# Kernel tuning notes

Measured on AMD Instinct MI355X. Metric: run time of the kernel, lower is better.

The kernel has to match this reference:

```python
import jax, jax.numpy as jnp
import numpy as np

EPS = 1e-8  # matches torch F.cosine_similarity default eps


def _flatten_spatial(x):
    # [B, C, d, h, w] -> [B, N, C]
    B, C = x.shape[:2]
    return x.reshape(B, C, -1).transpose(0, 2, 1)


def _stage_loss(canon_src, canon_tgt, src_desc, tgt_desc):
    stage_size = src_desc.shape[2:]
    B, C = canon_src.shape[:2]
    # trilinear resize with half-pixel centers == torch align_corners=False
    rs = jax.image.resize(canon_src, (B, C) + stage_size, method='trilinear')
    rt = jax.image.resize(canon_tgt, (B, C) + stage_size, method='trilinear')
    a = _flatten_spatial(rs)  # [B, N, 3]
    b = _flatten_spatial(rt)  # [B, N, 3]
    # squared euclidean distances (argmin is invariant to sqrt)
    a2 = jnp.sum(a * a, axis=-1)  # [B, N]
    b2 = jnp.sum(b * b, axis=-1)  # [B, N]
    ab = jnp.einsum('bnc,bmc->bnm', a, b)  # [B, N, N]
    d2 = a2[:, :, None] + b2[:, None, :] - 2.0 * ab
    nearest = jnp.argmin(d2, axis=-1)  # [B, N] int
    sd = _flatten_spatial(src_desc)  # [B, N, Cd]
    td = _flatten_spatial(tgt_desc)  # [B, N, Cd]
    gathered = jnp.take_along_axis(td, nearest[:, :, None], axis=1)  # [B, N, Cd]
    num = jnp.sum(sd * gathered, axis=-1)
    denom = jnp.maximum(jnp.linalg.norm(sd, axis=-1), EPS) * \
            jnp.maximum(jnp.linalg.norm(gathered, axis=-1), EPS)
    cos = num / denom
    return 1.0 - jnp.mean(cos)


def setup_inputs() -> dict:
    key = jax.random.key(0)
    ks = jax.random.split(key, 6)
    return {
        'canonical_source': jax.random.normal(ks[0], (4, 3, 64, 64, 64), jnp.float32),
        'canonical_target': jax.random.normal(ks[1], (4, 3, 64, 64, 64), jnp.float32),
        'src_desc0': jax.random.normal(ks[2], (4, 32, 16, 16, 16), jnp.float32),
        'tgt_desc0': jax.random.normal(ks[3], (4, 32, 16, 16, 16), jnp.float32),
        'src_desc1': jax.random.normal(ks[4], (4, 32, 8, 8, 8), jnp.float32),
        'tgt_desc1': jax.random.normal(ks[5], (4, 32, 8, 8, 8), jnp.float32),
    }


def reference(canonical_source, canonical_target, src_desc0, tgt_desc0, src_desc1, tgt_desc1):
    l0 = _stage_loss(canonical_source, canonical_target, src_desc0, tgt_desc0)
    l1 = _stage_loss(canonical_source, canonical_target, src_desc1, tgt_desc1)
    return jnp.stack([l0, l1]).mean()
```

## Files before the change

kernel.cpp:

```cpp
#include <hip/hip_runtime.h>
#include <cfloat>

typedef unsigned long long u64;

#define CDESC 32
#define N0 4096
#define N1 512

__device__ __forceinline__ unsigned fbits_mono(float d) {
    unsigned b = __float_as_uint(d);
    return (d >= 0.f) ? (b | 0x80000000u) : ~b;
}

__device__ __forceinline__ void wave_reduce_atomic(float v, float* acc) {
#pragma unroll
    for (int off = 32; off > 0; off >>= 1) v += __shfl_down(v, off, 64);
    if ((threadIdx.x & 63) == 0) atomicAdd(acc, v);
}

__global__ __launch_bounds__(256) void pass1_fused(
        const float* __restrict__ csrc, const float* __restrict__ ctgt,
        const float* __restrict__ sd0, const float* __restrict__ td0,
        const float* __restrict__ sd1, const float* __restrict__ td1,
        float* __restrict__ t16a, float* __restrict__ t16b,
        float* __restrict__ t8a,  float* __restrict__ t8b,
        float* __restrict__ sd0T, float* __restrict__ td0T,
        float* __restrict__ sd1T, float* __restrict__ td1T,
        float* __restrict__ acc) {
    __shared__ __align__(16) float sRow[65 * 64];
    const int tid = threadIdx.x;
    const int bx  = blockIdx.x, by = blockIdx.y;
    if (by == 0 && bx == 0 && tid < 4) acc[tid] = 0.f;

    if (bx < 768) {
        int bc = bx >> 6, z = bx & 63;
        const float* in = by ? ctgt : csrc;
        float* o16 = by ? t16b : t16a;
        float* o8  = by ? t8b  : t8a;
        const float4* src = (const float4*)(in + (size_t)(bc * 64 + z) * 4096);
#pragma unroll
        for (int k = 0; k < 4; ++k) {
            float4 v = src[tid + k * 256];
            int g = tid + k * 256;
            int y = g >> 4, j = (g & 15) * 4;
            float* p = &sRow[y * 65 + j];
            p[0] = v.x; p[1] = v.y; p[2] = v.z; p[3] = v.w;
        }
        __syncthreads();
#pragma unroll
        for (int k = 0; k < 6; ++k) {
            int o = tid + k * 256;
            if (o < 1024) {
                int y = o >> 4, xo = o & 15;
                int j0 = 4 * xo - 2;
                float sum = 0.f, wsum = 0.f;
#pragma unroll
                for (int t = 0; t < 8; ++t) {
                    int j = j0 + t;
                    float w = 1.f - fabsf((float)t - 3.5f) / 4.f;
                    if (j >= 0 && j < 64) { sum = fmaf(w, sRow[y * 65 + j], sum); wsum += w; }
                }
                o16[bc * 65536 + z * 1024 + y * 16 + xo] = sum / wsum;
            } else {
                int o2 = o - 1024;
                int y = o2 >> 3, xo = o2 & 7;
                int j0 = 8 * xo - 4;
                float sum = 0.f, wsum = 0.f;
#pragma unroll
                for (int t = 0; t < 16; ++t) {
                    int j = j0 + t;
                    float w = 1.f - fabsf((float)t - 7.5f) / 8.f;
                    if (j >= 0 && j < 64) { sum = fmaf(w, sRow[y * 65 + j], sum); wsum += w; }
                }
                o8[bc * 32768 + z * 512 + y * 8 + xo] = sum / wsum;
            }
        }
    } else {
        __shared__ float tile[64 * 33];
        int tl = bx - 768;
        const float* din; float* dout; int N, b, n0;
        if (tl < 256) { din = by ? td0 : sd0; dout = by ? td0T : sd0T;
                        N = N0; b = tl >> 6; n0 = (tl & 63) * 64; }
        else { tl -= 256; din = by ? td1 : sd1; dout = by ? td1T : sd1T;
               N = N1; b = tl >> 3; n0 = (tl & 7) * 64; }
#pragma unroll
        for (int i = 0; i < 8; ++i) {
            int idx = tid + i * 256;
            int c = idx >> 6, j = idx & 63;
            tile[j * 33 + c] = din[((size_t)b * CDESC + c) * N + n0 + j];
        }
        __syncthreads();
#pragma unroll
        for (int i = 0; i < 8; ++i) {
            int idx = tid + i * 256;
            int p = idx >> 5, c = idx & 31;
            dout[((size_t)b * N + n0 + p) * CDESC + c] = tile[p * 33 + c];
        }
    }
}

__global__ __launch_bounds__(256) void pass2_both(
        const float* __restrict__ t16a, const float* __restrict__ t16b,
        const float* __restrict__ t8a,  const float* __restrict__ t8b,
        float4* __restrict__ ps0, float4* __restrict__ pt0,
        float4* __restrict__ ps1, float4* __restrict__ pt1) {
    int gid = blockIdx.x * 256 + threadIdx.x;
    if (blockIdx.x < 1024) {
        int sub = gid & 7, p = gid >> 3;
        int side = p >> 14, r = p & 16383;
        int b = r >> 12, n = r & 4095;
        int x = n & 15, y = (n >> 4) & 15, z = n >> 8;
        const float* t = side ? t16b : t16a;
        float wy[8]; int jy[8];
        float wys = 0.f, wzs = 0.f;
#pragma unroll
        for (int tt = 0; tt < 8; ++tt) {
            float w = 1.f - fabsf((float)tt - 3.5f) * 0.25f;
            int j = 4 * y - 2 + tt;
            bool v = (unsigned)j < 64u;
            wy[tt] = v ? w : 0.f; jy[tt] = v ? j : 0; wys += wy[tt];
            int jz = 4 * z - 2 + tt;
            if ((unsigned)jz < 64u) wzs += w;
        }
        float a0 = 0.f, a1 = 0.f, a2 = 0.f;
        {
            float wz = 1.f - fabsf((float)sub - 3.5f) * 0.25f;
            int jz = 4 * z - 2 + sub;
            if ((unsigned)jz < 64u) {
                const float* bz = t + (size_t)b * 196608 + jz * 1024 + x;
#pragma unroll
                for (int ty = 0; ty < 8; ++ty) {
                    float w = wz * wy[ty];
                    const float* pr = bz + jy[ty] * 16;
                    a0 = fmaf(w, pr[0],      a0);
                    a1 = fmaf(w, pr[65536],  a1);
                    a2 = fmaf(w, pr[131072], a2);
                }
            }
        }
#pragma unroll
        for (int m = 1; m < 8; m <<= 1) {
            a0 += __shfl_xor(a0, m, 64);
            a1 += __shfl_xor(a1, m, 64);
            a2 += __shfl_xor(a2, m, 64);
        }
        if (sub == 0) {
            float inv = 1.f / (wys * wzs);
            a0 *= inv; a1 *= inv; a2 *= inv;
            float sq = a0 * a0 + a1 * a1 + a2 * a2;
            if (side) pt0[b * N0 + n] = make_float4(-2.f * a0, -2.f * a1, -2.f * a2, sq);
            else      ps0[b * N0 + n] = make_float4(a0, a1, a2, sq);
        }
    } else {
        int g = gid - 262144;
        int sub = g & 7, p = g >> 3;
        int side = p >> 11, r = p & 2047;
        int b = r >> 9, n = r & 511;
        int x = n & 7, y = (n >> 3) & 7, z = n >> 6;
        const float* t = side ? t8b : t8a;
        constexpr int CS = 64 * 64 * 8;
        float wy[16]; int jy[16];
        float wys = 0.f, wzs = 0.f;
#pragma unroll
        for (int tt = 0; tt < 16; ++tt) {
            float w = 1.f - fabsf((float)tt - 7.5f) * 0.125f;
            int j = 8 * y - 4 + tt;
            bool v = (unsigned)j < 64u;
            wy[tt] = v ? w : 0.f; jy[tt] = v ? j : 0; wys += wy[tt];
            int jz = 8 * z - 4 + tt;
            if ((unsigned)jz < 64u) wzs += w;
        }
        float a0 = 0.f, a1 = 0.f, a2 = 0.f;
#pragma unroll
        for (int k = 0; k < 2; ++k) {
            int tt = 2 * sub + k;
            float wz = 1.f - fabsf((float)tt - 7.5f) * 0.125f;
            int jz = 8 * z - 4 + tt;
            if ((unsigned)jz < 64u) {
                const float* bz = t + b * 3 * CS + jz * (64 * 8) + x;
#pragma unroll 1
                for (int ty = 0; ty < 16; ++ty) {
                    float w = wz * wy[ty];
                    const float* pr = bz + jy[ty] * 8;
                    a0 = fmaf(w, pr[0],      a0);
                    a1 = fmaf(w, pr[CS],     a1);
                    a2 = fmaf(w, pr[2 * CS], a2);
                }
            }
        }
#pragma unroll
        for (int m = 1; m < 8; m <<= 1) {
            a0 += __shfl_xor(a0, m, 64);
            a1 += __shfl_xor(a1, m, 64);
            a2 += __shfl_xor(a2, m, 64);
        }
        if (sub == 0) {
            float inv = 1.f / (wys * wzs);
            a0 *= inv; a1 *= inv; a2 *= inv;
            float sq = a0 * a0 + a1 * a1 + a2 * a2;
            if (side) pt1[b * N1 + n] = make_float4(-2.f * a0, -2.f * a1, -2.f * a2, sq);
            else      ps1[b * N1 + n] = make_float4(a0, a1, a2, sq);
        }
    }
}

__device__ __forceinline__ float cos_pm(const float* __restrict__ sT,
                                        const float* __restrict__ tT,
                                        size_t si, size_t ti) {
    const float4* s = (const float4*)(sT + si * CDESC);
    const float4* t = (const float4*)(tT + ti * CDESC);
    float num = 0.f, s2 = 0.f, t2 = 0.f;
#pragma unroll
    for (int c = 0; c < 8; ++c) {
        float4 a = s[c], g = t[c];
        num = fmaf(a.x, g.x, fmaf(a.y, g.y, fmaf(a.z, g.z, fmaf(a.w, g.w, num))));
        s2  = fmaf(a.x, a.x, fmaf(a.y, a.y, fmaf(a.z, a.z, fmaf(a.w, a.w, s2))));
        t2  = fmaf(g.x, g.x, fmaf(g.y, g.y, fmaf(g.z, g.z, fmaf(g.w, g.w, t2))));
    }
    return num / (fmaxf(sqrtf(s2), 1e-8f) * fmaxf(sqrtf(t2), 1e-8f));
}

__device__ __forceinline__ float dist_pm(float4 P, float4 Q) {
    return fmaf(P.x, Q.x, fmaf(P.y, Q.y, fmaf(P.z, Q.z, Q.w)));
}

__global__ __launch_bounds__(256) void nn_cos_all(
        const float4* __restrict__ ps0, const float4* __restrict__ pt0,
        const float* __restrict__ sd0T, const float* __restrict__ td0T,
        const float4* __restrict__ ps1, const float4* __restrict__ pt1,
        const float* __restrict__ sd1T, const float* __restrict__ td1T,
        float* acc, float* __restrict__ out) {
    extern __shared__ __align__(16) char smraw[];
    float4* sm = (float4*)smraw;
    const int tid = threadIdx.x;
    const int bx  = blockIdx.x;

    if (bx < 256) {
        int b = bx >> 6, ptile = bx & 63;
        const float4* tp = pt0 + b * N0;
        for (int i = tid; i < N0; i += 256)
            sm[i] = tp[i];
        __syncthreads();
        int w = tid >> 6, lane = tid & 63;
        int n = ptile * 64 + lane;
        float4 P = ps0[b * N0 + n];
        const int m0 = w * 1024;
        float best = FLT_MAX; int bbase = 0;
        for (int k0 = 0; k0 < 1024; k0 += 16) {
            float d[16];
#pragma unroll
            for (int u = 0; u < 16; ++u)
                d[u] = dist_pm(P, sm[m0 + k0 + u]);
            float e0 = fminf(d[0],  d[1]),  e1 = fminf(d[2],  d[3]);
            float e2 = fminf(d[4],  d[5]),  e3 = fminf(d[6],  d[7]);
            float e4 = fminf(d[8],  d[9]),  e5 = fminf(d[10], d[11]);
            float e6 = fminf(d[12], d[13]), e7 = fminf(d[14], d[15]);
            float f0 = fminf(e0, e1), f1 = fminf(e2, e3);
            float f2 = fminf(e4, e5), f3 = fminf(e6, e7);
            float bm = fminf(fminf(f0, f1), fminf(f2, f3));
            if (bm < best) { best = bm; bbase = k0; }
        }
        int bi = 0;
#pragma unroll
        for (int u = 15; u >= 0; --u) {
            float dv = dist_pm(P, sm[m0 + bbase + u]);
            if (dv == best) bi = u;
        }
        u64 key = ((u64)fbits_mono(best) << 32) | (unsigned)(m0 + bbase + bi);
        __syncthreads();
        u64* keys = (u64*)smraw;
        keys[w * 64 + lane] = key;
        __syncthreads();
        if (tid < 64) {
            u64 k0 = keys[tid],       k1 = keys[tid + 64];
            u64 k2 = keys[tid + 128], k3 = keys[tid + 192];
            u64 ka = k0 < k1 ? k0 : k1;
            u64 kb = k2 < k3 ? k2 : k3;
            u64 kk = ka < kb ? ka : kb;
            int nearest = (int)(unsigned)(kk & 0xFFFFFFFFull);
            int n2 = ptile * 64 + tid;
            float cosv = cos_pm(sd0T, td0T, (size_t)b * N0 + n2,
                                (size_t)b * N0 + nearest);
            wave_reduce_atomic(cosv, acc + 0);
        }
    } else {
        int bb = bx - 256;
        int b = bb >> 1;
        const float4* tp = pt1 + b * N1;
        for (int i = tid; i < N1; i += 256)
            sm[i] = tp[i];
        __syncthreads();
        int n = (bb & 1) * 256 + tid;
        float4 P = ps1[b * N1 + n];
        float best = FLT_MAX; int bbase = 0;
        for (int k0 = 0; k0 < N1; k0 += 16) {
            float d[16];
#pragma unroll
            for (int u = 0; u < 16; ++u)
                d[u] = dist_pm(P, sm[k0 + u]);
            float e0 = fminf(d[0],  d[1]),  e1 = fminf(d[2],  d[3]);
            float e2 = fminf(d[4],  d[5]),  e3 = fminf(d[6],  d[7]);
            float e4 = fminf(d[8],  d[9]),  e5 = fminf(d[10], d[11]);
            float e6 = fminf(d[12], d[13]), e7 = fminf(d[14], d[15]);
            float f0 = fminf(e0, e1), f1 = fminf(e2, e3);
            float f2 = fminf(e4, e5), f3 = fminf(e6, e7);
            float bm = fminf(fminf(f0, f1), fminf(f2, f3));
            if (bm < best) { best = bm; bbase = k0; }
        }
        int bi = 0;
#pragma unroll
        for (int u = 15; u >= 0; --u) {
            float dv = dist_pm(P, sm[bbase + u]);
            if (dv == best) bi = u;
        }
        float cosv = cos_pm(sd1T, td1T, (size_t)b * N1 + n,
                            (size_t)b * N1 + bbase + bi);
        wave_reduce_atomic(cosv, acc + 1);
    }

    __syncthreads();
    if (tid == 0) {
        __threadfence();
        unsigned old = atomicAdd((unsigned*)(acc + 2), 1u);
        if (old == 263u) {
            float a0 = atomicAdd(acc + 0, 0.f);
            float a1 = atomicAdd(acc + 1, 0.f);
            out[0] = 1.f - 0.5f * (a0 * (1.f / 16384.f) + a1 * (1.f / 2048.f));
        }
    }
}

extern "C" void kernel_launch(void* const* d_in, const int* in_sizes, int n_in,
                              void* d_out, int out_size, void* d_ws, size_t ws_size,
                              hipStream_t stream) {
    const float* c_src = (const float*)d_in[0];
    const float* c_tgt = (const float*)d_in[1];
    const float* sd0   = (const float*)d_in[2];
    const float* td0   = (const float*)d_in[3];
    const float* sd1   = (const float*)d_in[4];
    const float* td1   = (const float*)d_in[5];
    float* out = (float*)d_out;

    char* ws = (char*)d_ws;
    float* acc  = (float*)ws;
    float* t16a = (float*)(ws + 256);
    float* t16b = t16a + 786432;
    float* t8a  = t16b + 786432;
    float* t8b  = t8a + 393216;
    float4* ps0 = (float4*)(t8b + 393216);
    float4* pt0 = ps0 + 16384;
    float4* ps1 = pt0 + 16384;
    float4* pt1 = ps1 + 2048;
    float* sd0T = (float*)(pt1 + 2048);
    float* td0T = sd0T + 524288;
    float* sd1T = td0T + 524288;
    float* td1T = sd1T + 65536;

    pass1_fused<<<dim3(1056, 2), 256, 0, stream>>>(c_src, c_tgt, sd0, td0, sd1, td1,
                                                   t16a, t16b, t8a, t8b,
                                                   sd0T, td0T, sd1T, td1T, acc);
    pass2_both<<<1152, 256, 0, stream>>>(t16a, t16b, t8a, t8b, ps0, pt0, ps1, pt1);
    nn_cos_all<<<264, 256, 65536, stream>>>(ps0, pt0, sd0T, td0T, ps1, pt1,
                                            sd1T, td1T, acc, out);
}
```

Before: 125.3 us.

## Fuse Y-axis resize into first pass, leaving only Z-axis filtering for pass two

The first pass now does both the X and Y separable trilinear downsampling in shared memory for each z-slice, and writes only the XY-reduced intermediates. This shrinks those intermediates by a factor of four at 16^3 and eight at 8^3. The second pass then does a single Z-direction filter, one thread per output point, with far fewer blocks and no shuffle reduction. This cuts intermediate global traffic and second-pass work, at the cost of extra shared memory and a second barrier in the first pass.

```diff
diff --git a/kernel.cpp b/kernel.cpp
--- a/kernel.cpp
+++ b/kernel.cpp
@@ -22,12 +22,14 @@
         const float* __restrict__ csrc, const float* __restrict__ ctgt,
         const float* __restrict__ sd0, const float* __restrict__ td0,
         const float* __restrict__ sd1, const float* __restrict__ td1,
-        float* __restrict__ t16a, float* __restrict__ t16b,
-        float* __restrict__ t8a,  float* __restrict__ t8b,
+        float* __restrict__ x16a, float* __restrict__ x16b,
+        float* __restrict__ x8a,  float* __restrict__ x8b,
         float* __restrict__ sd0T, float* __restrict__ td0T,
         float* __restrict__ sd1T, float* __restrict__ td1T,
         float* __restrict__ acc) {
     __shared__ __align__(16) float sRow[65 * 64];
+    __shared__ float xf16[64 * 17];
+    __shared__ float xf8[64 * 9];
     const int tid = threadIdx.x;
     const int bx  = blockIdx.x, by = blockIdx.y;
     if (by == 0 && bx == 0 && tid < 4) acc[tid] = 0.f;
@@ -35,8 +37,8 @@
     if (bx < 768) {
         int bc = bx >> 6, z = bx & 63;
         const float* in = by ? ctgt : csrc;
-        float* o16 = by ? t16b : t16a;
-        float* o8  = by ? t8b  : t8a;
+        float* o16 = by ? x16b : x16a;
+        float* o8  = by ? x8b  : x8a;
         const float4* src = (const float4*)(in + (size_t)(bc * 64 + z) * 4096);
 #pragma unroll
         for (int k = 0; k < 4; ++k) {
@@ -60,7 +62,7 @@
                     float w = 1.f - fabsf((float)t - 3.5f) / 4.f;
                     if (j >= 0 && j < 64) { sum = fmaf(w, sRow[y * 65 + j], sum); wsum += w; }
                 }
-                o16[bc * 65536 + z * 1024 + y * 16 + xo] = sum / wsum;
+                xf16[y * 17 + xo] = sum / wsum;
             } else {
                 int o2 = o - 1024;
                 int y = o2 >> 3, xo = o2 & 7;
@@ -72,8 +74,33 @@
                     float w = 1.f - fabsf((float)t - 7.5f) / 8.f;
                     if (j >= 0 && j < 64) { sum = fmaf(w, sRow[y * 65 + j], sum); wsum += w; }
                 }
-                o8[bc * 32768 + z * 512 + y * 8 + xo] = sum / wsum;
-            }
+                xf8[y * 9 + xo] = sum / wsum;
+            }
+        }
+        __syncthreads();
+        {
+            int y2 = tid >> 4, x = tid & 15;
+            int j0 = 4 * y2 - 2;
+            float sum = 0.f, wsum = 0.f;
+#pragma unroll
+            for (int t = 0; t < 8; ++t) {
+                int j = j0 + t;
+                float w = 1.f - fabsf((float)t - 3.5f) / 4.f;
+                if (j >= 0 && j < 64) { sum = fmaf(w, xf16[j * 17 + x], sum); wsum += w; }
+            }
+            o16[bc * 16384 + z * 256 + y2 * 16 + x] = sum / wsum;
+        }
+        if (tid < 64) {
+            int y2 = tid >> 3, x = tid & 7;
+            int j0 = 8 * y2 - 4;
+            float sum = 0.f, wsum = 0.f;
+#pragma unroll
+            for (int t = 0; t < 16; ++t) {
+                int j = j0 + t;
+                float w = 1.f - fabsf((float)t - 7.5f) / 8.f;
+                if (j >= 0 && j < 64) { sum = fmaf(w, xf8[j * 9 + x], sum); wsum += w; }
+            }
+            o8[bc * 4096 + z * 64 + y2 * 8 + x] = sum / wsum;
         }
     } else {
         __shared__ float tile[64 * 33];
@@ -99,108 +126,61 @@
     }
 }
 
-__global__ __launch_bounds__(256) void pass2_both(
-        const float* __restrict__ t16a, const float* __restrict__ t16b,
-        const float* __restrict__ t8a,  const float* __restrict__ t8b,
+__global__ __launch_bounds__(256) void pass2z(
+        const float* __restrict__ x16a, const float* __restrict__ x16b,
+        const float* __restrict__ x8a,  const float* __restrict__ x8b,
         float4* __restrict__ ps0, float4* __restrict__ pt0,
         float4* __restrict__ ps1, float4* __restrict__ pt1) {
     int gid = blockIdx.x * 256 + threadIdx.x;
-    if (blockIdx.x < 1024) {
-        int sub = gid & 7, p = gid >> 3;
-        int side = p >> 14, r = p & 16383;
+    if (blockIdx.x < 128) {
+        int side = gid >> 14, r = gid & 16383;
         int b = r >> 12, n = r & 4095;
         int x = n & 15, y = (n >> 4) & 15, z = n >> 8;
-        const float* t = side ? t16b : t16a;
-        float wy[8]; int jy[8];
-        float wys = 0.f, wzs = 0.f;
+        const float* t = side ? x16b : x16a;
+        const float* base = t + (size_t)b * 49152 + y * 16 + x;
+        float a0 = 0.f, a1 = 0.f, a2 = 0.f, wzs = 0.f;
 #pragma unroll
         for (int tt = 0; tt < 8; ++tt) {
             float w = 1.f - fabsf((float)tt - 3.5f) * 0.25f;
-            int j = 4 * y - 2 + tt;
-            bool v = (unsigned)j < 64u;
-            wy[tt] = v ? w : 0.f; jy[tt] = v ? j : 0; wys += wy[tt];
             int jz = 4 * z - 2 + tt;
-            if ((unsigned)jz < 64u) wzs += w;
-        }
-        float a0 = 0.f, a1 = 0.f, a2 = 0.f;
-        {
-            float wz = 1.f - fabsf((float)sub - 3.5f) * 0.25f;
-            int jz = 4 * z - 2 + sub;
             if ((unsigned)jz < 64u) {
-                const float* bz = t + (size_t)b * 196608 + jz * 1024 + x;
-#pragma unroll
-                for (int ty = 0; ty < 8; ++ty) {
-                    float w = wz * wy[ty];
-                    const float* pr = bz + jy[ty] * 16;
-                    a0 = fmaf(w, pr[0],      a0);
-                    a1 = fmaf(w, pr[65536],  a1);
-                    a2 = fmaf(w, pr[131072], a2);
-                }
-            }
-        }
-#pragma unroll
-        for (int m = 1; m < 8; m <<= 1) {
-            a0 += __shfl_xor(a0, m, 64);
-            a1 += __shfl_xor(a1, m, 64);
-            a2 += __shfl_xor(a2, m, 64);
-        }
-        if (sub == 0) {
-            float inv = 1.f / (wys * wzs);
-            a0 *= inv; a1 *= inv; a2 *= inv;
-            float sq = a0 * a0 + a1 * a1 + a2 * a2;
-            if (side) pt0[b * N0 + n] = make_float4(-2.f * a0, -2.f * a1, -2.f * a2, sq);
-            else      ps0[b * N0 + n] = make_float4(a0, a1, a2, sq);
-        }
+                const float* p = base + jz * 256;
+                a0 = fmaf(w, p[0],     a0);
+                a1 = fmaf(w, p[16384], a1);
+                a2 = fmaf(w, p[32768], a2);
+                wzs += w;
+            }
+        }
+        float inv = 1.f / wzs;
+        a0 *= inv; a1 *= inv; a2 *= inv;
+        float sq = a0 * a0 + a1 * a1 + a2 * a2;
+        if (side) pt0[b * N0 + n] = make_float4(-2.f * a0, -2.f * a1, -2.f * a2, sq);
+        else      ps0[b * N0 + n] = make_float4(a0, a1, a2, sq);
     } else {
-        int g = gid - 262144;
-        int sub = g & 7, p = g >> 3;
-        int side = p >> 11, r = p & 2047;
+        int g = gid - 32768;
+        int side = g >> 11, r = g & 2047;
         int b = r >> 9, n = r & 511;
         int x = n & 7, y = (n >> 3) & 7, z = n >> 6;
-        const float* t = side ? t8b : t8a;
-        constexpr int CS = 64 * 64 * 8;
-        float wy[16]; int jy[16];
-        float wys = 0.f, wzs = 0.f;
+        const float* t = side ? x8b : x8a;
+        const float* base = t + (size_t)b * 12288 + y * 8 + x;
+        float a0 = 0.f, a1 = 0.f, a2 = 0.f, wzs = 0.f;
 #pragma unroll
         for (int tt = 0; tt < 16; ++tt) {
             float w = 1.f - fabsf((float)tt - 7.5f) * 0.125f;
-            int j = 8 * y - 4 + tt;
-            bool v = (unsigned)j < 64u;
-            wy[tt] = v ? w : 0.f; jy[tt] = v ? j : 0; wys += wy[tt];
-            int jz = 8 * z - 4 + tt;
-            if ((unsigned)jz < 64u) wzs += w;
-        }
-        float a0 = 0.f, a1 = 0.f, a2 = 0.f;
-#pragma unroll
-        for (int k = 0; k < 2; ++k) {
-            int tt = 2 * sub + k;
-            float wz = 1.f - fabsf((float)tt - 7.5f) * 0.125f;
             int jz = 8 * z - 4 + tt;
             if ((unsigned)jz < 64u) {
-                const float* bz = t + b * 3 * CS + jz * (64 * 8) + x;
-#pragma unroll 1
-                for (int ty = 0; ty < 16; ++ty) {
-                    float w = wz * wy[ty];
-                    const float* pr = bz + jy[ty] * 8;
-                    a0 = fmaf(w, pr[0],      a0);
-                    a1 = fmaf(w, pr[CS],     a1);
-                    a2 = fmaf(w, pr[2 * CS], a2);
-                }
-            }
-        }
-#pragma unroll
-        for (int m = 1; m < 8; m <<= 1) {
-            a0 += __shfl_xor(a0, m, 64);
-            a1 += __shfl_xor(a1, m, 64);
-            a2 += __shfl_xor(a2, m, 64);
-        }
-        if (sub == 0) {
-            float inv = 1.f / (wys * wzs);
-            a0 *= inv; a1 *= inv; a2 *= inv;
-            float sq = a0 * a0 + a1 * a1 + a2 * a2;
-            if (side) pt1[b * N1 + n] = make_float4(-2.f * a0, -2.f * a1, -2.f * a2, sq);
-            else      ps1[b * N1 + n] = make_float4(a0, a1, a2, sq);
-        }
+                const float* p = base + jz * 64;
+                a0 = fmaf(w, p[0],    a0);
+                a1 = fmaf(w, p[4096], a1);
+                a2 = fmaf(w, p[8192], a2);
+                wzs += w;
+            }
+        }
+        float inv = 1.f / wzs;
+        a0 *= inv; a1 *= inv; a2 *= inv;
+        float sq = a0 * a0 + a1 * a1 + a2 * a2;
+        if (side) pt1[b * N1 + n] = make_float4(-2.f * a0, -2.f * a1, -2.f * a2, sq);
+        else      ps1[b * N1 + n] = make_float4(a0, a1, a2, sq);
     }
 }
 
@@ -343,11 +323,11 @@
 
     char* ws = (char*)d_ws;
     float* acc  = (float*)ws;
-    float* t16a = (float*)(ws + 256);
-    float* t16b = t16a + 786432;
-    float* t8a  = t16b + 786432;
-    float* t8b  = t8a + 393216;
-    float4* ps0 = (float4*)(t8b + 393216);
+    float* x16a = (float*)(ws + 256);
+    float* x16b = x16a + 196608;
+    float* x8a  = x16b + 196608;
+    float* x8b  = x8a + 49152;
+    float4* ps0 = (float4*)(x8b + 49152);
     float4* pt0 = ps0 + 16384;
     float4* ps1 = pt0 + 16384;
     float4* pt1 = ps1 + 2048;
@@ -357,9 +337,9 @@
     float* td1T = sd1T + 65536;
 
     pass1_fused<<<dim3(1056, 2), 256, 0, stream>>>(c_src, c_tgt, sd0, td0, sd1, td1,
-                                                   t16a, t16b, t8a, t8b,
+                                                   x16a, x16b, x8a, x8b,
                                                    sd0T, td0T, sd1T, td1T, acc);
-    pass2_both<<<1152, 256, 0, stream>>>(t16a, t16b, t8a, t8b, ps0, pt0, ps1, pt1);
+    pass2z<<<144, 256, 0, stream>>>(x16a, x16b, x8a, x8b, ps0, pt0, ps1, pt1);
     nn_cos_all<<<264, 256, 65536, stream>>>(ps0, pt0, sd0T, td0T, ps1, pt1,
                                             sd1T, td1T, acc, out);
 }
```

Result: faster. 116.5 us (-7.0%).
